# Performance work log

Hardware: AMD Instinct MI355X
Metric: run time of the kernel (lower is better)

The kernel has to match this reference:

```python
import jax, jax.numpy as jnp
import numpy as np
import math

B, S, D, H, F = 4, 1024, 1024, 16, 4096
NUM_BUCKETS, MAX_DISTANCE = 32, 128
LN_EPS = 1e-5


def _relative_position_bucket(relative_position, num_buckets=NUM_BUCKETS, max_distance=MAX_DISTANCE):
    # bidirectional T5 bucketing, faithful to the torch source
    n = -relative_position
    num_buckets = num_buckets // 2  # 16
    ret = (n < 0).astype(jnp.int32) * num_buckets
    n = jnp.abs(n)
    max_exact = num_buckets // 2  # 8
    is_small = n < max_exact
    val_if_large = max_exact + (
        jnp.log(jnp.maximum(n, 1).astype(jnp.float32) / max_exact)
        / math.log(max_distance / max_exact)
        * (num_buckets - max_exact)
    ).astype(jnp.int32)
    val_if_large = jnp.minimum(val_if_large, num_buckets - 1)
    return ret + jnp.where(is_small, n, val_if_large)


def layer_norm(x, g, b):
    mu = jnp.mean(x, axis=-1, keepdims=True)
    var = jnp.mean((x - mu) ** 2, axis=-1, keepdims=True)
    return g * (x - mu) / jnp.sqrt(var + LN_EPS) + b


def setup_inputs() -> dict:
    key = jax.random.key(0)
    ks = jax.random.split(key, 12)
    s = 0.02
    return {
        "in_state": jax.random.normal(ks[0], (B, S, D), jnp.float32),
        "padding_mask": jnp.ones((B, S), jnp.int32),
        "Wq": jax.random.normal(ks[1], (D, D), jnp.float32) * s,
        "bq": jnp.zeros((D,), jnp.float32),
        "Wk": jax.random.normal(ks[2], (D, D), jnp.float32) * s,
        "bk": jnp.zeros((D,), jnp.float32),
        "Wv": jax.random.normal(ks[3], (D, D), jnp.float32) * s,
        "bv": jnp.zeros((D,), jnp.float32),
        "Wo": jax.random.normal(ks[4], (D, D), jnp.float32) * s,
        "bo": jnp.zeros((D,), jnp.float32),
        "rel_bias": jax.random.normal(ks[5], (NUM_BUCKETS, H), jnp.float32) * s,
        "ln1_g": jnp.ones((D,), jnp.float32),
        "ln1_b": jnp.zeros((D,), jnp.float32),
        "W1": jax.random.normal(ks[6], (D, F), jnp.float32) * s,
        "b1": jnp.zeros((F,), jnp.float32),
        "W2": jax.random.normal(ks[7], (F, D), jnp.float32) * s,
        "b2": jnp.zeros((D,), jnp.float32),
        "ln2_g": jnp.ones((D,), jnp.float32),
        "ln2_b": jnp.zeros((D,), jnp.float32),
    }


def reference(in_state, padding_mask, Wq, bq, Wk, bk, Wv, bv, Wo, bo, rel_bias,
              ln1_g, ln1_b, W1, b1, W2, b2, ln2_g, ln2_b):
    b, s, d = in_state.shape
    dh = d // H
    q = in_state @ Wq + bq
    k = in_state @ Wk + bk
    v = in_state @ Wv + bv
    # faithful to torch's q.view(B*H, S, d_head) flat reshape (no head transpose)
    qh = q.reshape(b * H, s, dh)
    kh = k.reshape(b * H, s, dh)
    vh = v.reshape(b * H, s, dh)
    scores = jnp.einsum('bqd,bkd->bqk', qh, kh)  # no 1/sqrt(d) scaling (T5 style)
    # relative position bias: [H, S, S] tiled over batch -> block index b*H+h gets head h
    rel_pos = jnp.arange(s)[:, None] - jnp.arange(s)[None, :]
    buckets = _relative_position_bucket(rel_pos)
    bias = rel_bias[buckets].transpose(2, 0, 1)  # [H, S, S]
    bias = jnp.tile(bias, (b, 1, 1))  # [B*H, S, S]
    # padding mask: log(0/1) -> -inf/0; block b*H+h uses mask[b, value_index]
    pad = jnp.log(padding_mask.astype(jnp.float32))  # [B, S]
    pad = jnp.repeat(pad, H, axis=0)[:, None, :]  # [B*H, 1, S]
    attw = jax.nn.softmax(scores + bias + pad, axis=-1)
    att = (attw @ vh).reshape(b, s, d)
    att = att @ Wo + bo
    h = layer_norm(att + in_state, ln1_g, ln1_b)
    ff = jnp.maximum(h @ W1 + b1, 0.0) @ W2 + b2
    out = layer_norm(ff + h, ln2_g, ln2_b)
    return out
```

## Files before the change

### kernel.cpp

```cpp
#include <hip/hip_runtime.h>
#include <hip/hip_bf16.h>

typedef unsigned short u16;
typedef __attribute__((ext_vector_type(8))) short bhalf8;
typedef __attribute__((ext_vector_type(4))) float f32x4;

#define DEV __device__ __forceinline__

DEV float bf2f(u16 u) { union { unsigned int i; float f; } c; c.i = ((unsigned int)u) << 16; return c.f; }
DEV u16 f2bf(float f) {
  union { float f; unsigned int i; } c; c.f = f;
  unsigned int x = c.i;
  x += 0x7fffu + ((x >> 16) & 1u);
  return (u16)(x >> 16);
}

DEV void async16(const void* g, void* l) {
  __builtin_amdgcn_global_load_lds((__attribute__((address_space(1))) void*)g,
                                   (__attribute__((address_space(3))) void*)l, 16, 0, 0);
}

struct Ptr11 { const void* p[11]; };
struct TC4 { const void* in[4]; u16* out[4]; };

__global__ void detect_kernel(const unsigned int* __restrict__ x, int* __restrict__ flag) {
  int t = threadIdx.x;
  int cnt = 0;
  for (int i = t; i < 256; i += 64) {
    unsigned int w = x[i];
    int e = (w >> 7) & 0xFF;
    if (e >= 96 && e <= 134) cnt++;
  }
#pragma unroll
  for (int o = 1; o < 64; o <<= 1) cnt += __shfl_xor(cnt, o, 64);
  if (t == 0) *flag = (cnt >= 192) ? 1 : 0;
}

DEV bhalf8 load8B(const void* base, size_t e, int isbf) {
  if (isbf) return *(const bhalf8*)((const u16*)base + e);
  const float* f = (const float*)base + e;
  float4 a = *(const float4*)f;
  float4 b = *(const float4*)(f + 4);
  bhalf8 r;
  r[0] = (short)f2bf(a.x); r[1] = (short)f2bf(a.y); r[2] = (short)f2bf(a.z); r[3] = (short)f2bf(a.w);
  r[4] = (short)f2bf(b.x); r[5] = (short)f2bf(b.y); r[6] = (short)f2bf(b.z); r[7] = (short)f2bf(b.w);
  return r;
}

__global__ __launch_bounds__(256) void convert_x(const void* __restrict__ x,
                                                 u16* __restrict__ dst,
                                                 const int* __restrict__ flag) {
  int c = blockIdx.x * 256 + threadIdx.x;
  u16* d = dst + (size_t)c * 4;
  if (*flag) {
    *(ushort4*)d = ((const ushort4*)x)[c];
  } else {
    float4 v = ((const float4*)x)[c];
    d[0] = f2bf(v.x); d[1] = f2bf(v.y); d[2] = f2bf(v.z); d[3] = f2bf(v.w);
  }
}

__global__ __launch_bounds__(256) void convert_small(Ptr11 s, float* __restrict__ dst,
                                                     const int* __restrict__ flag) {
  const int isbf = *flag;
  const int SZ[11] = {1024,1024,1024,1024,512,1024,1024,4096,1024,1024,1024};
  for (int i = threadIdx.x; i < 13824; i += 256) {
    int acc = 0, seg = -1, off = 0;
#pragma unroll
    for (int s2 = 0; s2 < 11; ++s2) {
      if (seg < 0 && i < acc + SZ[s2]) { seg = s2; off = i - acc; }
      acc += SZ[s2];
    }
    dst[i] = isbf ? bf2f(((const u16*)s.p[seg])[off]) : ((const float*)s.p[seg])[off];
  }
}

DEV void tconv_tile(const void* in, u16* out, int R, int C, int isbf) {
  __shared__ __align__(16) u16 tile[64][72];
  const int t = threadIdx.x;
  const int c0 = blockIdx.x * 64, r0 = blockIdx.y * 64;
#pragma unroll
  for (int r = 0; r < 2; ++r) {
    int idx = r * 256 + t;
    int ri = idx >> 3, cc = (idx & 7) * 8;
    bhalf8 v = load8B(in, (size_t)(r0 + ri) * C + c0 + cc, isbf);
    *(bhalf8*)(&tile[ri][cc]) = v;
  }
  __syncthreads();
#pragma unroll
  for (int r = 0; r < 2; ++r) {
    int idx = r * 256 + t;
    int co = idx >> 3, rc = (idx & 7) * 8;
    bhalf8 v;
#pragma unroll
    for (int ii = 0; ii < 8; ++ii) v[ii] = (short)tile[rc + ii][co];
    *(bhalf8*)(out + (size_t)(c0 + co) * R + r0 + rc) = v;
  }
}

__global__ __launch_bounds__(256) void tconv_w4(TC4 p, const int* __restrict__ flag) {
  int z = blockIdx.z;
  tconv_tile(p.in[z], p.out[z], 1024, 1024, *flag);
}

__global__ __launch_bounds__(256) void tconv_generic(const void* in, u16* out, int R, int C,
                                                     const int* __restrict__ flag) {
  tconv_tile(in, out, R, C, *flag);
}

__global__ __launch_bounds__(256) void transpose_generic(const u16* in, u16* out, int R, int C) {
  __shared__ __align__(16) u16 tile[64][72];
  const int t = threadIdx.x;
  const int c0 = blockIdx.x * 64, r0 = blockIdx.y * 64;
  size_t bs = (size_t)R * C * blockIdx.z;
#pragma unroll
  for (int r = 0; r < 2; ++r) {
    int idx = r * 256 + t;
    int ri = idx >> 3, cc = (idx & 7) * 8;
    *(bhalf8*)(&tile[ri][cc]) = *(const bhalf8*)(in + bs + (size_t)(r0 + ri) * C + c0 + cc);
  }
  __syncthreads();
#pragma unroll
  for (int r = 0; r < 2; ++r) {
    int idx = r * 256 + t;
    int co = idx >> 3, rc = (idx & 7) * 8;
    bhalf8 v;
#pragma unroll
    for (int ii = 0; ii < 8; ++ii) v[ii] = (short)tile[rc + ii][co];
    *(bhalf8*)(out + bs + (size_t)(c0 + co) * R + r0 + rc) = v;
  }
}

template<int RELU>
__global__ __launch_bounds__(512) void gemm_bt(
    const u16* __restrict__ A, const u16* __restrict__ BT0,
    const float* __restrict__ b0, const float* __restrict__ b1, const float* __restrict__ b2,
    u16* __restrict__ C0, int M, int N, int K, long sBT, long sC)
{
  __shared__ __align__(16) u16 ldsA[128 * 32];
  __shared__ __align__(16) u16 ldsB[128 * 32];

  const int t = threadIdx.x;
  const int wv = t >> 6, l = t & 63;
  const int wm = wv >> 2, wn = wv & 3;
  const int m0 = blockIdx.y * 128, n0 = blockIdx.x * 128;
  const int z = blockIdx.z;

  const u16* BT = BT0 + (long)z * sBT;
  const float* bias = (z == 0) ? b0 : (z == 1 ? b1 : b2);
  u16* C = C0 + (long)z * sC;

  const int mm_s = t >> 2, kc_s = (t & 3) ^ ((t >> 4) & 3);
  const u16* agp = A + (size_t)(m0 + mm_s) * K + kc_s * 8;
  const u16* bgp = BT + (size_t)(n0 + mm_s) * K + kc_s * 8;
  char* la = (char*)ldsA + wv * 1024;
  char* lb = (char*)ldsB + wv * 1024;

  int a_off[4], b_off[2];
#pragma unroll
  for (int i = 0; i < 4; ++i) {
    int mm = wm * 64 + i * 16 + (l & 15);
    a_off[i] = (mm * 4 + ((l >> 4) ^ ((mm >> 2) & 3))) * 8;
  }
#pragma unroll
  for (int j = 0; j < 2; ++j) {
    int nn = wn * 32 + j * 16 + (l & 15);
    b_off[j] = (nn * 4 + ((l >> 4) ^ ((nn >> 2) & 3))) * 8;
  }

  f32x4 acc[4][2] = {};

  for (int kt = 0; kt < K; kt += 32) {
    __syncthreads();
    async16(agp + kt, la);
    async16(bgp + kt, lb);
    __syncthreads();

    bhalf8 af[4], bfr[2];
#pragma unroll
    for (int i = 0; i < 4; ++i) af[i] = *(const bhalf8*)(ldsA + a_off[i]);
#pragma unroll
    for (int j = 0; j < 2; ++j) bfr[j] = *(const bhalf8*)(ldsB + b_off[j]);
#pragma unroll
    for (int mi = 0; mi < 4; ++mi)
#pragma unroll
      for (int nj = 0; nj < 2; ++nj)
        acc[mi][nj] = __builtin_amdgcn_mfma_f32_16x16x32_bf16(af[mi], bfr[nj], acc[mi][nj], 0, 0, 0);
  }

  const int lr = (l >> 4) << 2, lc = l & 15;
#pragma unroll
  for (int nj = 0; nj < 2; ++nj) {
    int col = n0 + wn * 32 + nj * 16 + lc;
    float bb = bias[col];
#pragma unroll
    for (int mi = 0; mi < 4; ++mi) {
#pragma unroll
      for (int r = 0; r < 4; ++r) {
        int row = m0 + wm * 64 + mi * 16 + lr + r;
        float v = acc[mi][nj][r] + bb;
        if (RELU) v = fmaxf(v, 0.0f);
        C[(size_t)row * N + col] = f2bf(v);
      }
    }
  }
}

template<int RELU>
__global__ __launch_bounds__(256) void gemm_bn(
    const u16* __restrict__ A, const void* __restrict__ B,
    const float* __restrict__ bias, u16* __restrict__ C, int M, int N, int K,
    const int* __restrict__ flag)
{
  __shared__ __align__(16) u16 ldsA[128][40];
  __shared__ __align__(16) u16 ldsB[128][40];

  const int isbf = *flag;
  const int t = threadIdx.x;
  const int wv = t >> 6, l = t & 63;
  const int wm = wv & 1, wn = wv >> 1;
  const int m0 = blockIdx.y * 128, n0 = blockIdx.x * 128;

  const int srow = t >> 1, scol = (t & 1) * 16;
  const u16* agp = A + (size_t)(m0 + srow) * K + scol;

  const int kk = t >> 3;
  const int nn = (t & 7) * 16;

  f32x4 acc[4][4] = {};

  for (int kt = 0; kt < K; kt += 32) {
    bhalf8 a0 = *(const bhalf8*)(agp + kt);
    bhalf8 a1 = *(const bhalf8*)(agp + kt + 8);
    size_t e0 = (size_t)(kt + kk) * N + n0 + nn;
    bhalf8 b0v = load8B(B, e0, isbf);
    bhalf8 b1v = load8B(B, e0 + 8, isbf);
    __syncthreads();
    *(bhalf8*)(&ldsA[srow][scol])     = a0;
    *(bhalf8*)(&ldsA[srow][scol + 8]) = a1;
#pragma unroll
    for (int j = 0; j < 8; ++j) ldsB[nn + j][kk]     = (u16)b0v[j];
#pragma unroll
    for (int j = 0; j < 8; ++j) ldsB[nn + 8 + j][kk] = (u16)b1v[j];
    __syncthreads();

    bhalf8 af[4], bfr[4];
#pragma unroll
    for (int i = 0; i < 4; ++i)
      af[i] = *(const bhalf8*)(&ldsA[wm * 64 + i * 16 + (l & 15)][(l >> 4) * 8]);
#pragma unroll
    for (int i = 0; i < 4; ++i)
      bfr[i] = *(const bhalf8*)(&ldsB[wn * 64 + i * 16 + (l & 15)][(l >> 4) * 8]);
#pragma unroll
    for (int mi = 0; mi < 4; ++mi)
#pragma unroll
      for (int ni = 0; ni < 4; ++ni)
        acc[mi][ni] = __builtin_amdgcn_mfma_f32_16x16x32_bf16(af[mi], bfr[ni], acc[mi][ni], 0, 0, 0);
  }

  const int lr = (l >> 4) << 2, lc = l & 15;
#pragma unroll
  for (int ni = 0; ni < 4; ++ni) {
    int col = n0 + wn * 64 + ni * 16 + lc;
    float bb = bias[col];
#pragma unroll
    for (int mi = 0; mi < 4; ++mi) {
#pragma unroll
      for (int r = 0; r < 4; ++r) {
        int row = m0 + wm * 64 + mi * 16 + lr + r;
        float v = acc[mi][ni][r] + bb;
        if (RELU) v = fmaxf(v, 0.0f);
        C[(size_t)row * N + col] = f2bf(v);
      }
    }
  }
}

__global__ __launch_bounds__(256) void lut_kernel(const float* __restrict__ rbc, float* __restrict__ lut) {
  int idx = blockIdx.x * 256 + threadIdx.x;
  if (idx >= 16 * 2047) return;
  int h = idx / 2047;
  int dp = idx - h * 2047;
  int delta = dp - 1023;
  int n = -delta;
  int ret = 0;
  if (n < 0) { ret = 16; n = -n; }
  int bkt;
  if (n < 8) bkt = n;
  else {
    float v = logf((float)n * 0.125f) / logf(16.0f) * 8.0f;
    bkt = 8 + (int)v;
    if (bkt > 15) bkt = 15;
  }
  lut[idx] = (rbc[(ret + bkt) * 16 + h] - 12.0f) * 1.44269504f;
}

__global__ __launch_bounds__(256) void attn_fused(
    const u16* __restrict__ q, const u16* __restrict__ k, const u16* __restrict__ vt,
    const int* __restrict__ mask, const float* __restrict__ lut, u16* __restrict__ att)
{
  __shared__ __align__(16) u16 ldsQ[64][72];
  __shared__ __align__(16) u16 ldsK[64][72];
  __shared__ __align__(16) u16 ldsV[64][72];
  __shared__ __align__(16) u16 ldsP[4][16][72];
  __shared__ float ldsLut[2047];
  __shared__ float ldsPad[64];

  const int t = threadIdx.x;
  const int wv = t >> 6, l = t & 63;
  const int bh = blockIdx.x, qt = blockIdx.y;
  const int b = bh >> 4, h = bh & 15;
  const size_t base = (size_t)bh * 65536;
  const int q0 = qt * 64;

  for (int i = t; i < 2047; i += 256) ldsLut[i] = lut[h * 2047 + i];

  const int sr = t >> 2, sc = (t & 3) * 16;
  {
    bhalf8 q0v = *(const bhalf8*)(q + base + (size_t)(q0 + sr) * 64 + sc);
    bhalf8 q1v = *(const bhalf8*)(q + base + (size_t)(q0 + sr) * 64 + sc + 8);
    *(bhalf8*)(&ldsQ[sr][sc])     = q0v;
    *(bhalf8*)(&ldsQ[sr][sc + 8]) = q1v;
  }
  __syncthreads();

  bhalf8 qf[2];
  {
    int mm = wv * 16 + (l & 15);
#pragma unroll
    for (int s = 0; s < 2; ++s)
      qf[s] = *(const bhalf8*)(&ldsQ[mm][s * 32 + (l >> 4) * 8]);
  }

  float ls_part[4] = {0.0f, 0.0f, 0.0f, 0.0f};
  f32x4 acc_o[4] = {};

  const int* mrow = mask + b * 1024;

  for (int kt = 0; kt < 16; ++kt) {
    const int k0 = kt * 64;
    bhalf8 k0v = *(const bhalf8*)(k + base + (size_t)(k0 + sr) * 64 + sc);
    bhalf8 k1v = *(const bhalf8*)(k + base + (size_t)(k0 + sr) * 64 + sc + 8);
    bhalf8 v0v = *(const bhalf8*)(vt + base + (size_t)sr * 1024 + k0 + sc);
    bhalf8 v1v = *(const bhalf8*)(vt + base + (size_t)sr * 1024 + k0 + sc + 8);
    __syncthreads();
    *(bhalf8*)(&ldsK[sr][sc])     = k0v;
    *(bhalf8*)(&ldsK[sr][sc + 8]) = k1v;
    *(bhalf8*)(&ldsV[sr][sc])     = v0v;
    *(bhalf8*)(&ldsV[sr][sc + 8]) = v1v;
    if (t < 64) {
      int mv = mrow[k0 + t];
      ldsPad[t] = (mv > 0) ? __log2f((float)mv) : -1e30f;
    }
    __syncthreads();

    f32x4 accS[4] = {};
#pragma unroll
    for (int s = 0; s < 2; ++s) {
#pragma unroll
      for (int ni = 0; ni < 4; ++ni) {
        int nnj = ni * 16 + (l & 15);
        bhalf8 kf = *(const bhalf8*)(&ldsK[nnj][s * 32 + (l >> 4) * 8]);
        accS[ni] = __builtin_amdgcn_mfma_f32_16x16x32_bf16(qf[s], kf, accS[ni], 0, 0, 0);
      }
    }

    float padv[4];
#pragma unroll
    for (int ni = 0; ni < 4; ++ni) padv[ni] = ldsPad[ni * 16 + (l & 15)];
    const int ib = q0 + wv * 16 + ((l >> 4) << 2);
#pragma unroll
    for (int r = 0; r < 4; ++r) {
      int i_l = ((l >> 4) << 2) + r;
#pragma unroll
      for (int ni = 0; ni < 4; ++ni) {
        int j_l = ni * 16 + (l & 15);
        float s = fmaf(accS[ni][r], 1.44269504f, ldsLut[(ib + r) - (k0 + j_l) + 1023]) + padv[ni];
        float p = exp2f(s);
        ls_part[r] += p;
        ldsP[wv][i_l][j_l] = f2bf(p);
      }
    }

#pragma unroll
    for (int s = 0; s < 2; ++s) {
      int mm = l & 15;
      bhalf8 pf = *(const bhalf8*)(&ldsP[wv][mm][s * 32 + (l >> 4) * 8]);
#pragma unroll
      for (int ni = 0; ni < 4; ++ni) {
        int e = ni * 16 + (l & 15);
        bhalf8 vf = *(const bhalf8*)(&ldsV[e][s * 32 + (l >> 4) * 8]);
        acc_o[ni] = __builtin_amdgcn_mfma_f32_16x16x32_bf16(pf, vf, acc_o[ni], 0, 0, 0);
      }
    }
  }

#pragma unroll
  for (int r = 0; r < 4; ++r) {
#pragma unroll
    for (int off = 1; off < 16; off <<= 1) ls_part[r] += __shfl_xor(ls_part[r], off, 64);
    ls_part[r] = 1.0f / ls_part[r];
  }

#pragma unroll
  for (int ni = 0; ni < 4; ++ni) {
#pragma unroll
    for (int r = 0; r < 4; ++r) {
      int i = q0 + wv * 16 + ((l >> 4) << 2) + r;
      int e = ni * 16 + (l & 15);
      att[base + (size_t)i * 64 + e] = f2bf(acc_o[ni][r] * ls_part[r]);
    }
  }
}

template<int LAST>
__global__ __launch_bounds__(256) void ln_kernel(
    const u16* __restrict__ x, const u16* __restrict__ res,
    const float* __restrict__ g, const float* __restrict__ b,
    void* __restrict__ out, const int* __restrict__ flag)
{
  const int row = blockIdx.x, t = threadIdx.x;
  const size_t off = (size_t)row * 1024 + t * 4;
  ushort4 xv = *(const ushort4*)(x + off);
  ushort4 rv = *(const ushort4*)(res + off);
  float v0 = bf2f(xv.x) + bf2f(rv.x);
  float v1 = bf2f(xv.y) + bf2f(rv.y);
  float v2 = bf2f(xv.z) + bf2f(rv.z);
  float v3 = bf2f(xv.w) + bf2f(rv.w);
  float s = v0 + v1 + v2 + v3;
  float sq = v0 * v0 + v1 * v1 + v2 * v2 + v3 * v3;
#pragma unroll
  for (int o = 1; o < 64; o <<= 1) { s += __shfl_xor(s, o, 64); sq += __shfl_xor(sq, o, 64); }
  __shared__ float red[8];
  const int wv = t >> 6, l = t & 63;
  if (l == 0) { red[wv] = s; red[4 + wv] = sq; }
  __syncthreads();
  s = red[0] + red[1] + red[2] + red[3];
  sq = red[4] + red[5] + red[6] + red[7];
  float mu = s * 0.0009765625f;
  float var = sq * 0.0009765625f - mu * mu;
  float rstd = rsqrtf(var + 1e-5f);
  float4 gv = *(const float4*)(g + t * 4);
  float4 bv = *(const float4*)(b + t * 4);
  float o0 = gv.x * (v0 - mu) * rstd + bv.x;
  float o1 = gv.y * (v1 - mu) * rstd + bv.y;
  float o2 = gv.z * (v2 - mu) * rstd + bv.z;
  float o3 = gv.w * (v3 - mu) * rstd + bv.w;
  if (!LAST) {
    ushort4 ov; ov.x = f2bf(o0); ov.y = f2bf(o1); ov.z = f2bf(o2); ov.w = f2bf(o3);
    *(ushort4*)((u16*)out + off) = ov;
  } else {
    if (*flag) {
      ushort4 ov; ov.x = f2bf(o0); ov.y = f2bf(o1); ov.z = f2bf(o2); ov.w = f2bf(o3);
      *(ushort4*)((u16*)out + off) = ov;
    } else {
      float4 ov; ov.x = o0; ov.y = o1; ov.z = o2; ov.w = o3;
      *(float4*)((float*)out + off) = ov;
    }
  }
}

extern "C" void kernel_launch(void* const* d_in, const int* in_sizes, int n_in,
                              void* d_out, int out_size, void* d_ws, size_t ws_size,
                              hipStream_t stream) {
  const void* x  = d_in[0];
  const int* mask = (const int*)d_in[1];
  const void* Wq = d_in[2];  const void* bq = d_in[3];
  const void* Wk = d_in[4];  const void* bk = d_in[5];
  const void* Wv = d_in[6];  const void* bv = d_in[7];
  const void* Wo = d_in[8];  const void* bo = d_in[9];
  const void* rb = d_in[10];
  const void* g1 = d_in[11]; const void* be1 = d_in[12];
  const void* W1 = d_in[13]; const void* b1 = d_in[14];
  const void* W2 = d_in[15]; const void* b2 = d_in[16];
  const void* g2 = d_in[17]; const void* be2 = d_in[18];

  char* ws = (char*)d_ws;
  const size_t MB = 1024 * 1024;
  const bool FAST = (ws_size >= 57 * MB);

  const size_t TAIL = FAST ? 56 * MB : 48 * MB;
  float* smalls = (float*)(ws + TAIL);
  float* lut    = (float*)(ws + TAIL + 56 * 1024);
  int*   flag   = (int*)(ws + TAIL + 192 * 1024);

  float* bqc  = smalls + 0;
  float* bkc  = smalls + 1024;
  float* bvc  = smalls + 2048;
  float* boc  = smalls + 3072;
  float* rbc  = smalls + 4096;
  float* g1c  = smalls + 4608;
  float* be1c = smalls + 5632;
  float* b1c  = smalls + 6656;
  float* b2c  = smalls + 10752;
  float* g2c  = smalls + 11776;
  float* be2c = smalls + 12800;

  detect_kernel<<<1, 64, 0, stream>>>((const unsigned int*)x, flag);
  Ptr11 sml;
  sml.p[0] = bq; sml.p[1] = bk; sml.p[2] = bv; sml.p[3] = bo; sml.p[4] = rb;
  sml.p[5] = g1; sml.p[6] = be1; sml.p[7] = b1; sml.p[8] = b2; sml.p[9] = g2; sml.p[10] = be2;
  convert_small<<<1, 256, 0, stream>>>(sml, smalls, flag);
  lut_kernel<<<dim3(128), 256, 0, stream>>>(rbc, lut);

  if (FAST) {
    u16* xc   = (u16*)(ws + 0 * MB);
    u16* WqT  = (u16*)(ws + 8 * MB);
    u16* WkT  = WqT + 1048576;
    u16* WvT  = WqT + 2 * 1048576;
    u16* WoT  = WqT + 3 * 1048576;
    u16* qb   = (u16*)(ws + 16 * MB);
    u16* kb   = (u16*)(ws + 24 * MB);
    u16* vb   = (u16*)(ws + 32 * MB);
    u16* vtb  = (u16*)(ws + 40 * MB);
    u16* attb = (u16*)(ws + 32 * MB);
    u16* xo   = (u16*)(ws + 16 * MB);
    u16* hb   = (u16*)(ws + 48 * MB);
    u16* W1T  = (u16*)(ws + 8 * MB);
    u16* W2T  = (u16*)(ws + 0 * MB);
    u16* ff1  = (u16*)(ws + 16 * MB);
    u16* ff2o = (u16*)(ws + 8 * MB);

    convert_x<<<4096, 256, 0, stream>>>(x, xc, flag);
    TC4 tw; tw.in[0] = Wq; tw.in[1] = Wk; tw.in[2] = Wv; tw.in[3] = Wo;
    tw.out[0] = WqT; tw.out[1] = WkT; tw.out[2] = WvT; tw.out[3] = WoT;
    tconv_w4<<<dim3(16, 16, 4), 256, 0, stream>>>(tw, flag);

    gemm_bt<0><<<dim3(8, 32, 3), 512, 0, stream>>>(xc, WqT, bqc, bkc, bvc, qb,
                                                   4096, 1024, 1024, 1048576L, 4194304L);
    transpose_generic<<<dim3(1, 16, 64), 256, 0, stream>>>(vb, vtb, 1024, 64);
    attn_fused<<<dim3(64, 16), 256, 0, stream>>>(qb, kb, vtb, mask, lut, attb);
    gemm_bt<0><<<dim3(8, 32, 1), 512, 0, stream>>>(attb, WoT, boc, boc, boc, xo,
                                                   4096, 1024, 1024, 0L, 0L);
    tconv_generic<<<dim3(64, 16), 256, 0, stream>>>(W1, W1T, 1024, 4096, flag);
    ln_kernel<0><<<dim3(4096), 256, 0, stream>>>(xo, xc, g1c, be1c, hb, flag);
    tconv_generic<<<dim3(16, 64), 256, 0, stream>>>(W2, W2T, 4096, 1024, flag);
    gemm_bt<1><<<dim3(32, 32, 1), 512, 0, stream>>>(hb, W1T, b1c, b1c, b1c, ff1,
                                                    4096, 4096, 1024, 0L, 0L);
    gemm_bt<0><<<dim3(8, 32, 1), 512, 0, stream>>>(ff1, W2T, b2c, b2c, b2c, ff2o,
                                                   4096, 1024, 4096, 0L, 0L);
    ln_kernel<1><<<dim3(4096), 256, 0, stream>>>(ff2o, hb, g2c, be2c, d_out, flag);
  } else {
    u16* xc   = (u16*)(ws + 0 * MB);
    u16* WqT  = (u16*)(ws + 8 * MB);
    u16* WkT  = WqT + 1048576;
    u16* WvT  = WqT + 2 * 1048576;
    u16* WoT  = WqT + 3 * 1048576;
    u16* qb   = (u16*)(ws + 16 * MB);
    u16* kb   = (u16*)(ws + 24 * MB);
    u16* vb   = (u16*)(ws + 32 * MB);
    u16* vtb  = (u16*)(ws + 40 * MB);
    u16* attb = (u16*)(ws + 32 * MB);
    u16* xo   = (u16*)(ws + 16 * MB);
    u16* hb   = (u16*)(ws + 40 * MB);
    u16* ff1  = (u16*)(ws + 0 * MB);
    u16* ff2o = (u16*)(ws + 32 * MB);

    convert_x<<<4096, 256, 0, stream>>>(x, xc, flag);
    TC4 tw; tw.in[0] = Wq; tw.in[1] = Wk; tw.in[2] = Wv; tw.in[3] = Wo;
    tw.out[0] = WqT; tw.out[1] = WkT; tw.out[2] = WvT; tw.out[3] = WoT;
    tconv_w4<<<dim3(16, 16, 4), 256, 0, stream>>>(tw, flag);

    gemm_bt<0><<<dim3(8, 32, 3), 512, 0, stream>>>(xc, WqT, bqc, bkc, bvc, qb,
                                                   4096, 1024, 1024, 1048576L, 4194304L);
    transpose_generic<<<dim3(1, 16, 64), 256, 0, stream>>>(vb, vtb, 1024, 64);
    attn_fused<<<dim3(64, 16), 256, 0, stream>>>(qb, kb, vtb, mask, lut, attb);
    gemm_bt<0><<<dim3(8, 32, 1), 512, 0, stream>>>(attb, WoT, boc, boc, boc, xo,
                                                   4096, 1024, 1024, 0L, 0L);
    ln_kernel<0><<<dim3(4096), 256, 0, stream>>>(xo, xc, g1c, be1c, hb, flag);
    gemm_bn<1><<<dim3(32, 32), 256, 0, stream>>>(hb, W1, b1c, ff1, 4096, 4096, 1024, flag);
    gemm_bn<0><<<dim3(8, 32), 256, 0, stream>>>(ff1, W2, b2c, ff2o, 4096, 1024, 4096, flag);
    ln_kernel<1><<<dim3(4096), 256, 0, stream>>>(ff2o, hb, g2c, be2c, d_out, flag);
  }
}
```

Measured before the change: 451.9 us.

## Add 256x256-tile pipelined GEMM kernel for QKV and FFN1 projections

Adds a new bf16 MFMA GEMM with 256x256 block tiles and 64-wide K steps, double-buffered in 128KB of LDS. Global-to-LDS async loads are interleaved with four MFMA quadrant phases, and s_setprio raises wave priority during the math. It replaces the 128x128 kernel for the QKV projection and the first FFN GEMM, raising data reuse per tile and hiding load latency. The cost is fewer blocks, which hurts occupancy and wave-count balance (192 and 256 blocks), plus heavy register and LDS use.

```diff
diff --git a/kernel.cpp b/kernel.cpp
--- a/kernel.cpp
+++ b/kernel.cpp
@@ -128,6 +128,176 @@
 #pragma unroll
     for (int ii = 0; ii < 8; ++ii) v[ii] = (short)tile[rc + ii][co];
     *(bhalf8*)(out + bs + (size_t)(c0 + co) * R + r0 + rc) = v;
+  }
+}
+
+#define MFMA_BF16(a, b, c) __builtin_amdgcn_mfma_f32_16x16x32_bf16(a, b, c, 0, 0, 0)
+
+template<int RELU>
+__global__ __launch_bounds__(512) void gemm256(
+    const u16* __restrict__ A, const u16* __restrict__ BT0,
+    const float* __restrict__ b0, const float* __restrict__ b1, const float* __restrict__ b2,
+    u16* __restrict__ C0, int M, int N, int K, long sBT, long sC)
+{
+  __shared__ __align__(16) u16 ldsAll[65536];
+  (void)M;
+
+  const int t = threadIdx.x;
+  const int wv = t >> 6, l = t & 63;
+  const int wm = wv >> 2, wn = wv & 3;
+  const int m0 = blockIdx.y * 256, n0 = blockIdx.x * 256;
+  const int z = blockIdx.z;
+
+  const u16* BT = BT0 + (long)z * sBT;
+  const float* bias = (z == 0) ? b0 : (z == 1 ? b1 : b2);
+  u16* C = C0 + (long)z * sC;
+
+  const int ri = t >> 3;
+  const int slc8 = (((t & 7) ^ (ri & 7)) << 3);
+  const u16* agp = A + (size_t)(m0 + ri) * K + slc8;
+  const int rB = ((ri >> 5) << 6) | (ri & 31);
+  const u16* bgp = BT + (size_t)(n0 + rB) * K + slc8;
+
+  char* lbase = (char*)ldsAll;
+  char* ldst = lbase + wv * 1024;
+
+#define STG_A(bufb, h, j, kt) async16(agp + (size_t)((j) * 128 + (h) * 64) * K + (size_t)(kt) * 64, \
+                                      ldst + (bufb) * 32768 + (h) * 16384 + (j) * 8192)
+#define STG_B(bufb, h, j, kt) async16(bgp + (size_t)((j) * 128 + (h) * 32) * K + (size_t)(kt) * 64, \
+                                      ldst + 65536 + (bufb) * 32768 + (h) * 16384 + (j) * 8192)
+
+  int offA[4][2], offB[2][2];
+#pragma unroll
+  for (int mi = 0; mi < 4; ++mi)
+#pragma unroll
+    for (int s = 0; s < 2; ++s)
+      offA[mi][s] = wm * 8192 + (mi * 16 + (l & 15)) * 128 + ((((s << 2) + (l >> 4)) ^ (l & 7)) << 4);
+#pragma unroll
+  for (int nj = 0; nj < 2; ++nj)
+#pragma unroll
+    for (int s = 0; s < 2; ++s)
+      offB[nj][s] = 65536 + wn * 4096 + (nj * 16 + (l & 15)) * 128 + ((((s << 2) + (l >> 4)) ^ (l & 7)) << 4);
+
+  const int NT = K >> 6;
+  f32x4 acc[8][4] = {};
+
+  STG_A(0, 0, 0, 0); STG_A(0, 0, 1, 0);
+  STG_B(0, 0, 0, 0); STG_B(0, 0, 1, 0);
+  STG_B(0, 1, 0, 0); STG_B(0, 1, 1, 0);
+  STG_A(0, 1, 0, 0); STG_A(0, 1, 1, 0);
+  if (NT > 1) {
+    STG_A(1, 0, 0, 1); STG_A(1, 0, 1, 1);
+    STG_B(1, 0, 0, 1); STG_B(1, 0, 1, 1);
+    STG_B(1, 1, 0, 1); STG_B(1, 1, 1, 1);
+    asm volatile("s_waitcnt vmcnt(6)" ::: "memory");
+  } else {
+    asm volatile("s_waitcnt vmcnt(0)" ::: "memory");
+  }
+  __builtin_amdgcn_s_barrier();
+
+  for (int tt = 0; tt < NT; ++tt) {
+    const int bf = tt & 1;
+    const int bo = bf << 15;
+    bhalf8 af[4][2], p0[2][2], p1[2][2];
+
+#pragma unroll
+    for (int mi = 0; mi < 4; ++mi)
+#pragma unroll
+      for (int s = 0; s < 2; ++s)
+        af[mi][s] = *(const bhalf8*)(lbase + bo + offA[mi][s]);
+#pragma unroll
+    for (int nj = 0; nj < 2; ++nj)
+#pragma unroll
+      for (int s = 0; s < 2; ++s)
+        p0[nj][s] = *(const bhalf8*)(lbase + bo + offB[nj][s]);
+    if (tt + 1 < NT) { STG_A(bf ^ 1, 1, 0, tt + 1); STG_A(bf ^ 1, 1, 1, tt + 1); }
+    __builtin_amdgcn_s_barrier();
+    asm volatile("s_waitcnt lgkmcnt(0)" ::: "memory");
+    __builtin_amdgcn_s_setprio(1);
+#pragma unroll
+    for (int mi = 0; mi < 4; ++mi)
+#pragma unroll
+      for (int nj = 0; nj < 2; ++nj) {
+        acc[mi][nj] = MFMA_BF16(af[mi][0], p0[nj][0], acc[mi][nj]);
+        acc[mi][nj] = MFMA_BF16(af[mi][1], p0[nj][1], acc[mi][nj]);
+      }
+    __builtin_amdgcn_s_setprio(0);
+    __builtin_amdgcn_s_barrier();
+
+#pragma unroll
+    for (int nj = 0; nj < 2; ++nj)
+#pragma unroll
+      for (int s = 0; s < 2; ++s)
+        p1[nj][s] = *(const bhalf8*)(lbase + bo + 16384 + offB[nj][s]);
+    if (tt + 2 < NT) { STG_A(bf, 0, 0, tt + 2); STG_A(bf, 0, 1, tt + 2); }
+    __builtin_amdgcn_s_barrier();
+    asm volatile("s_waitcnt lgkmcnt(0)" ::: "memory");
+    __builtin_amdgcn_s_setprio(1);
+#pragma unroll
+    for (int mi = 0; mi < 4; ++mi)
+#pragma unroll
+      for (int nj = 0; nj < 2; ++nj) {
+        acc[mi][2 + nj] = MFMA_BF16(af[mi][0], p1[nj][0], acc[mi][2 + nj]);
+        acc[mi][2 + nj] = MFMA_BF16(af[mi][1], p1[nj][1], acc[mi][2 + nj]);
+      }
+    __builtin_amdgcn_s_setprio(0);
+    __builtin_amdgcn_s_barrier();
+
+#pragma unroll
+    for (int mi = 0; mi < 4; ++mi)
+#pragma unroll
+      for (int s = 0; s < 2; ++s)
+        af[mi][s] = *(const bhalf8*)(lbase + bo + 16384 + offA[mi][s]);
+    if (tt + 2 < NT) { STG_B(bf, 0, 0, tt + 2); STG_B(bf, 0, 1, tt + 2); }
+    __builtin_amdgcn_s_barrier();
+    asm volatile("s_waitcnt lgkmcnt(0)" ::: "memory");
+    __builtin_amdgcn_s_setprio(1);
+#pragma unroll
+    for (int mi = 0; mi < 4; ++mi)
+#pragma unroll
+      for (int nj = 0; nj < 2; ++nj) {
+        acc[4 + mi][2 + nj] = MFMA_BF16(af[mi][0], p1[nj][0], acc[4 + mi][2 + nj]);
+        acc[4 + mi][2 + nj] = MFMA_BF16(af[mi][1], p1[nj][1], acc[4 + mi][2 + nj]);
+      }
+    __builtin_amdgcn_s_setprio(0);
+    __builtin_amdgcn_s_barrier();
+
+    if (tt + 2 < NT) { STG_B(bf, 1, 0, tt + 2); STG_B(bf, 1, 1, tt + 2); }
+    __builtin_amdgcn_s_barrier();
+    __builtin_amdgcn_s_setprio(1);
+#pragma unroll
+    for (int mi = 0; mi < 4; ++mi)
+#pragma unroll
+      for (int nj = 0; nj < 2; ++nj) {
+        acc[4 + mi][nj] = MFMA_BF16(af[mi][0], p0[nj][0], acc[4 + mi][nj]);
+        acc[4 + mi][nj] = MFMA_BF16(af[mi][1], p0[nj][1], acc[4 + mi][nj]);
+      }
+    __builtin_amdgcn_s_setprio(0);
+    if (tt < NT - 2) {
+      asm volatile("s_waitcnt vmcnt(6)" ::: "memory");
+    } else if (tt == NT - 2) {
+      asm volatile("s_waitcnt vmcnt(0)" ::: "memory");
+    }
+    __builtin_amdgcn_s_barrier();
+  }
+#undef STG_A
+#undef STG_B
+
+  const int lr = (l >> 4) << 2, lcc = l & 15;
+#pragma unroll
+  for (int nj = 0; nj < 4; ++nj) {
+    int col = n0 + wn * 64 + nj * 16 + lcc;
+    float bb = bias[col];
+#pragma unroll
+    for (int mi = 0; mi < 8; ++mi) {
+#pragma unroll
+      for (int r = 0; r < 4; ++r) {
+        int row = m0 + wm * 128 + mi * 16 + lr + r;
+        float v = acc[mi][nj][r] + bb;
+        if (RELU) v = fmaxf(v, 0.0f);
+        C[(size_t)row * N + col] = f2bf(v);
+      }
+    }
   }
 }
 
@@ -526,7 +696,7 @@
     tw.out[0] = WqT; tw.out[1] = WkT; tw.out[2] = WvT; tw.out[3] = WoT;
     tconv_w4<<<dim3(16, 16, 4), 256, 0, stream>>>(tw, flag);
 
-    gemm_bt<0><<<dim3(8, 32, 3), 512, 0, stream>>>(xc, WqT, bqc, bkc, bvc, qb,
+    gemm256<0><<<dim3(4, 16, 3), 512, 0, stream>>>(xc, WqT, bqc, bkc, bvc, qb,
                                                    4096, 1024, 1024, 1048576L, 4194304L);
     transpose_generic<<<dim3(1, 16, 64), 256, 0, stream>>>(vb, vtb, 1024, 64);
     attn_fused<<<dim3(64, 16), 256, 0, stream>>>(qb, kb, vtb, mask, lut, attb);
@@ -535,7 +705,7 @@
     tconv_generic<<<dim3(64, 16), 256, 0, stream>>>(W1, W1T, 1024, 4096, flag);
     ln_kernel<0><<<dim3(4096), 256, 0, stream>>>(xo, xc, g1c, be1c, hb, flag);
     tconv_generic<<<dim3(16, 64), 256, 0, stream>>>(W2, W2T, 4096, 1024, flag);
-    gemm_bt<1><<<dim3(32, 32, 1), 512, 0, stream>>>(hb, W1T, b1c, b1c, b1c, ff1,
+    gemm256<1><<<dim3(16, 16, 1), 512, 0, stream>>>(hb, W1T, b1c, b1c, b1c, ff1,
                                                     4096, 4096, 1024, 0L, 0L);
     gemm_bt<0><<<dim3(8, 32, 1), 512, 0, stream>>>(ff1, W2T, b2c, b2c, b2c, ff2o,
                                                    4096, 1024, 4096, 0L, 0L);
```

Result: faster. 436.9 us (-3.3%).
